# Kernel optimization log

Measured on AMD Instinct MI355X. Metric: run time of the kernel, lower is better.

Reference implementation:

```python
import jax, jax.numpy as jnp
import numpy as np

N_BUF = 60000.0
S_INIT = 2.0
S_INV = N_BUF ** S_INIT          # buffer init: N**S_init
S_HAT = (N_BUF ** 2) / S_INV     # == 1.0 at init


def setup_inputs() -> dict:
    key = jax.random.key(0)
    k1, k2 = jax.random.split(key)
    feats = jax.random.normal(k1, (16384, 128), dtype=jnp.float32)
    idx = jax.random.randint(k2, (16384,), 0, 60000).astype(jnp.int64)
    return {"feats": feats, "idx": idx}


def reference(feats, idx):
    # CauchyLoss.forward, faithful to the torch source. Note: the original
    # uses out-of-place masked_fill whose result is discarded, so neither the
    # diagonal nor the positive pairs are zeroed before the row-sum; we
    # replicate that exactly.
    n = feats.shape[0]
    B = n // 2
    sq = jnp.sum(feats * feats, axis=1)                      # [2B]
    d2 = sq[:, None] + sq[None, :] - 2.0 * (feats @ feats.T)  # [2B, 2B]
    d2 = jnp.maximum(d2, 0.0)
    q = 1.0 / (d2 + 1.0)                                      # [2B, 2B]
    # positive pairs: pos_mask = roll(eye(2B), B, dims=1) -> (i, (i+B) % 2B)
    rows = jnp.arange(n)
    qii = q[rows, (rows + B) % n]                             # [2B]
    attractive = -jnp.log(qii)
    repulsive = jnp.log(jnp.sum(q, axis=1)) * S_HAT           # [2B]
    return attractive.mean() + repulsive.mean()
```

## Files before the change

### kernel.cpp

```cpp
#include <hip/hip_runtime.h>
#include <hip/hip_bf16.h>

#define N 16384
#define D 128
#define NTI 128
#define GBLK 2112
#define B_HALF 8192

typedef __attribute__((ext_vector_type(8))) short short8;
typedef __attribute__((ext_vector_type(4))) float f32x4;

__device__ inline unsigned short f2bf(float x) {
    union { float f; unsigned u; } c; c.f = x;
    unsigned r = c.u + 0x7fffu + ((c.u >> 16) & 1u);
    return (unsigned short)(r >> 16);
}

__global__ __launch_bounds__(256)
void prep_kernel(const float* __restrict__ feats, unsigned short* __restrict__ fbP,
                 float* __restrict__ sq, float* __restrict__ rsum,
                 float* __restrict__ qii) {
    const int g  = blockIdx.x * 256 + threadIdx.x;
    const int p  = g >> 3;
    const int t8 = g & 7;
    const int i0 = p, i1 = p + B_HALF;
    const float4* ra = reinterpret_cast<const float4*>(feats + (size_t)i0 * D + t8 * 16);
    const float4* rb = reinterpret_cast<const float4*>(feats + (size_t)i1 * D + t8 * 16);
    char* da = (char*)fbP + (size_t)(i0 >> 7) * 32768 + (size_t)(i0 & 127) * 16;
    char* db = (char*)fbP + (size_t)(i1 >> 7) * 32768 + (size_t)(i1 & 127) * 16;
    float sa = 0.f, sb = 0.f, dot = 0.f;
#pragma unroll
    for (int c = 0; c < 2; ++c) {
        float4 x0 = ra[2 * c], x1 = ra[2 * c + 1];
        float4 y0 = rb[2 * c], y1 = rb[2 * c + 1];
        sa  += x0.x * x0.x + x0.y * x0.y + x0.z * x0.z + x0.w * x0.w
             + x1.x * x1.x + x1.y * x1.y + x1.z * x1.z + x1.w * x1.w;
        sb  += y0.x * y0.x + y0.y * y0.y + y0.z * y0.z + y0.w * y0.w
             + y1.x * y1.x + y1.y * y1.y + y1.z * y1.z + y1.w * y1.w;
        dot += x0.x * y0.x + x0.y * y0.y + x0.z * y0.z + x0.w * y0.w
             + x1.x * y1.x + x1.y * y1.y + x1.z * y1.z + x1.w * y1.w;
        short8 ca, cb;
        ca[0] = f2bf(x0.x); ca[1] = f2bf(x0.y); ca[2] = f2bf(x0.z); ca[3] = f2bf(x0.w);
        ca[4] = f2bf(x1.x); ca[5] = f2bf(x1.y); ca[6] = f2bf(x1.z); ca[7] = f2bf(x1.w);
        cb[0] = f2bf(y0.x); cb[1] = f2bf(y0.y); cb[2] = f2bf(y0.z); cb[3] = f2bf(y0.w);
        cb[4] = f2bf(y1.x); cb[5] = f2bf(y1.y); cb[6] = f2bf(y1.z); cb[7] = f2bf(y1.w);
        *reinterpret_cast<short8*>(da + (2 * t8 + c) * 2048) = ca;
        *reinterpret_cast<short8*>(db + (2 * t8 + c) * 2048) = cb;
    }
    sa  += __shfl_xor(sa, 1);  sa  += __shfl_xor(sa, 2);  sa  += __shfl_xor(sa, 4);
    sb  += __shfl_xor(sb, 1);  sb  += __shfl_xor(sb, 2);  sb  += __shfl_xor(sb, 4);
    dot += __shfl_xor(dot, 1); dot += __shfl_xor(dot, 2); dot += __shfl_xor(dot, 4);
    if (t8 == 0) {
        sq[i0] = sa; sq[i1] = sb;
        rsum[i0] = 0.f; rsum[i1] = 0.f;
        float d2 = fmaxf(sa + sb - 2.f * dot, 0.f);
        float q = 1.f / (d2 + 1.f);
        qii[i0] = q; qii[i1] = q;
    }
}

__device__ __forceinline__ void stage_panel(unsigned short* dst, const char* src,
                                            int wid, int lane) {
#pragma unroll
    for (int it = 0; it < 8; ++it) {
        const int lbase = it * 4096 + wid * 1024;
        __builtin_amdgcn_global_load_lds(
            (const __attribute__((address_space(1))) void*)(src + lbase + lane * 16),
            (__attribute__((address_space(3))) void*)((char*)dst + lbase), 16, 0, 0);
    }
}

__global__ __launch_bounds__(256, 2)
void gram_kernel(const unsigned short* __restrict__ fbP, const float* __restrict__ sq,
                 float* __restrict__ rsum) {
    __shared__ __align__(16) unsigned short lB[2][16 * 128 * 8];

    const int bid = (blockIdx.x & 7) * (GBLK / 8) + (blockIdx.x >> 3);

    int u = (int)((130.0f - sqrtf(16900.0f - 8.0f * (float)bid)) * 0.25f);
    if (u < 0) u = 0; if (u > 31) u = 31;
    while (u > 0 && 2 * u * (65 - u) > bid) --u;
    while (2 * (u + 1) * (64 - u) <= bid) ++u;
    int rem = bid - 2 * u * (65 - u);
    const int cnt = 32 - u;
    int sub = 0;
    while (rem >= cnt) { rem -= cnt; ++sub; }
    const int ti  = 4 * u + sub;
    const int tj0 = ti + 4 * rem;
    const int nt  = (NTI - tj0 < 4) ? (NTI - tj0) : 4;

    const int tid  = threadIdx.x;
    const int lane = tid & 63;
    const int wid  = tid >> 6;
    const int wr   = wid >> 1, wc = wid & 1;
    const int lrow = lane & 15;
    const int lk   = lane >> 4;

    const char* pa = (const char*)fbP + (size_t)ti * 32768;
    short8 a[4][4];
#pragma unroll
    for (int kk = 0; kk < 4; ++kk)
#pragma unroll
        for (int m = 0; m < 4; ++m)
            a[kk][m] = *reinterpret_cast<const short8*>(
                pa + (kk * 4 + lk) * 2048 + (wr * 64 + m * 16 + lrow) * 16);

    float sqa[4][4];
#pragma unroll
    for (int m = 0; m < 4; ++m) {
        const float4 v = *reinterpret_cast<const float4*>(
            sq + ti * 128 + wr * 64 + m * 16 + lk * 4);
        sqa[m][0] = v.x; sqa[m][1] = v.y; sqa[m][2] = v.z; sqa[m][3] = v.w;
    }
    float sqb1[4][4];
#pragma unroll
    for (int t = 0; t < 4; ++t)
        if (t < nt)
#pragma unroll
            for (int n = 0; n < 4; ++n)
                sqb1[t][n] = sq[(tj0 + t) * 128 + wc * 64 + n * 16 + lrow] + 1.0f;

    float racc[4][4];
#pragma unroll
    for (int m = 0; m < 4; ++m)
#pragma unroll
        for (int r = 0; r < 4; ++r) racc[m][r] = 0.f;

    stage_panel(lB[0], (const char*)fbP + (size_t)tj0 * 32768, wid, lane);

#pragma unroll
    for (int t = 0; t < 4; ++t) {
        if (t < nt) {
            if (t == 0) asm volatile("s_waitcnt vmcnt(0)" ::: "memory");
            else        asm volatile("s_waitcnt vmcnt(4)" ::: "memory");
            __builtin_amdgcn_sched_barrier(0);
            __builtin_amdgcn_s_barrier();

            if (t + 1 < nt)
                stage_panel(lB[(t + 1) & 1],
                            (const char*)fbP + (size_t)(tj0 + t + 1) * 32768, wid, lane);

            const char* lbuf = (const char*)lB[t & 1];
            f32x4 acc[4][4];
#pragma unroll
            for (int m = 0; m < 4; ++m)
#pragma unroll
                for (int n = 0; n < 4; ++n) acc[m][n] = (f32x4){0.f, 0.f, 0.f, 0.f};
#pragma unroll
            for (int kk = 0; kk < 4; ++kk) {
                short8 b[4];
#pragma unroll
                for (int n = 0; n < 4; ++n)
                    b[n] = *reinterpret_cast<const short8*>(
                        lbuf + (kk * 4 + lk) * 2048 + (wc * 64 + n * 16 + lrow) * 16);
#pragma unroll
                for (int m = 0; m < 4; ++m)
#pragma unroll
                    for (int n = 0; n < 4; ++n)
                        acc[m][n] = __builtin_amdgcn_mfma_f32_16x16x32_bf16(
                            a[kk][m], b[n], acc[m][n], 0, 0, 0);
            }

            float cloc[4] = {0.f, 0.f, 0.f, 0.f};
#pragma unroll
            for (int m = 0; m < 4; ++m)
#pragma unroll
                for (int n = 0; n < 4; ++n)
#pragma unroll
                    for (int r = 0; r < 4; ++r) {
                        float x = fmaf(-2.f, acc[m][n][r], sqa[m][r]);
                        float q = __builtin_amdgcn_rcpf(fmaxf(x + sqb1[t][n], 1.0f));
                        racc[m][r] += q;
                        cloc[n] += q;
                    }
            if (tj0 + t != ti) {
#pragma unroll
                for (int n = 0; n < 4; ++n) {
                    float v = cloc[n];
                    v += __shfl_xor(v, 16);
                    v += __shfl_xor(v, 32);
                    if (lane < 16)
                        atomicAdd(&rsum[(tj0 + t) * 128 + wc * 64 + n * 16 + lrow], v);
                }
            }
        }
    }

#pragma unroll
    for (int m = 0; m < 4; ++m)
#pragma unroll
        for (int r = 0; r < 4; ++r) {
            float v = racc[m][r];
            v += __shfl_xor(v, 1);
            v += __shfl_xor(v, 2);
            v += __shfl_xor(v, 4);
            v += __shfl_xor(v, 8);
            if (lrow == 0)
                atomicAdd(&rsum[ti * 128 + wr * 64 + m * 16 + lk * 4 + r], v);
        }
}

__global__ __launch_bounds__(256)
void finish1_kernel(const float* __restrict__ rsum, const float* __restrict__ qii,
                    float* __restrict__ partial) {
    __shared__ float red[4];
    const int i = blockIdx.x * 256 + threadIdx.x;
    float v = __logf(rsum[i]) - __logf(qii[i]);
#pragma unroll
    for (int m = 32; m >= 1; m >>= 1) v += __shfl_xor(v, m);
    if ((threadIdx.x & 63) == 0) red[threadIdx.x >> 6] = v;
    __syncthreads();
    if (threadIdx.x == 0) partial[blockIdx.x] = red[0] + red[1] + red[2] + red[3];
}

__global__ __launch_bounds__(64)
void finish2_kernel(const float* __restrict__ partial, unsigned* __restrict__ out) {
    float v = partial[threadIdx.x];
#pragma unroll
    for (int m = 32; m >= 1; m >>= 1) v += __shfl_xor(v, m);
    if (threadIdx.x == 0) {
        float val = v / (float)N;
        union { float f; unsigned u; } c; c.f = val;
        out[0] = (c.u & 0xFFFF0000u) | (unsigned)f2bf(val);
    }
}

extern "C" void kernel_launch(void* const* d_in, const int* in_sizes, int n_in,
                              void* d_out, int out_size, void* d_ws, size_t ws_size,
                              hipStream_t stream) {
    const float* feats = (const float*)d_in[0];
    char* ws = (char*)d_ws;
    unsigned short* fbP = (unsigned short*)ws;
    float* sq      = (float*)(ws + (size_t)N * D * 2);
    float* rsum    = (float*)(ws + (size_t)N * D * 2 + (size_t)N * 4);
    float* qii     = (float*)(ws + (size_t)N * D * 2 + (size_t)N * 8);
    float* partial = (float*)(ws + (size_t)N * D * 2 + (size_t)N * 12);

    hipLaunchKernelGGL(prep_kernel, dim3(256), dim3(256), 0, stream,
                       feats, fbP, sq, rsum, qii);
    hipLaunchKernelGGL(gram_kernel, dim3(GBLK), dim3(256), 0, stream,
                       fbP, sq, rsum);
    hipLaunchKernelGGL(finish1_kernel, dim3(64), dim3(256), 0, stream,
                       rsum, qii, partial);
    hipLaunchKernelGGL(finish2_kernel, dim3(1), dim3(64), 0, stream,
                       partial, (unsigned*)d_out);
}
```

Baseline: 91.31 us.

## Use 512-thread gram blocks with half-K panel staging and LDS column sums

Doubles the gram kernel block to 8 waves, so each wave owns a 32-row slice instead of 64 and holds half the A fragments and accumulators. The B panel is streamed in half-K chunks through a smaller double-buffered LDS area, and the per-tile sq values are loaded into LDS. Column partial sums are accumulated with LDS atomics and flushed to global once per block, and the MFMA loop is wrapped in s_setprio. The aim is higher occupancy and fewer global atomics, at the cost of twice as many barriers per tile and a full vmcnt(0) wait before each chunk.

```diff
diff --git a/kernel.cpp b/kernel.cpp
--- a/kernel.cpp
+++ b/kernel.cpp
@@ -59,21 +59,12 @@
     }
 }
 
-__device__ __forceinline__ void stage_panel(unsigned short* dst, const char* src,
-                                            int wid, int lane) {
-#pragma unroll
-    for (int it = 0; it < 8; ++it) {
-        const int lbase = it * 4096 + wid * 1024;
-        __builtin_amdgcn_global_load_lds(
-            (const __attribute__((address_space(1))) void*)(src + lbase + lane * 16),
-            (__attribute__((address_space(3))) void*)((char*)dst + lbase), 16, 0, 0);
-    }
-}
-
-__global__ __launch_bounds__(256, 2)
+__global__ __launch_bounds__(512, 4)
 void gram_kernel(const unsigned short* __restrict__ fbP, const float* __restrict__ sq,
                  float* __restrict__ rsum) {
-    __shared__ __align__(16) unsigned short lB[2][16 * 128 * 8];
+    __shared__ __align__(16) unsigned short lB[2][8 * 128 * 8];
+    __shared__ float cs[512];
+    __shared__ float sqL[512];
 
     const int bid = (blockIdx.x & 7) * (GBLK / 8) + (blockIdx.x >> 3);
 
@@ -92,102 +83,142 @@
     const int tid  = threadIdx.x;
     const int lane = tid & 63;
     const int wid  = tid >> 6;
-    const int wr   = wid >> 1, wc = wid & 1;
+    const int wr   = wid >> 1;
+    const int wc   = wid & 1;
     const int lrow = lane & 15;
     const int lk   = lane >> 4;
 
     const char* pa = (const char*)fbP + (size_t)ti * 32768;
-    short8 a[4][4];
+    short8 a[4][2];
 #pragma unroll
     for (int kk = 0; kk < 4; ++kk)
 #pragma unroll
-        for (int m = 0; m < 4; ++m)
+        for (int m = 0; m < 2; ++m)
             a[kk][m] = *reinterpret_cast<const short8*>(
-                pa + (kk * 4 + lk) * 2048 + (wr * 64 + m * 16 + lrow) * 16);
-
-    float sqa[4][4];
-#pragma unroll
-    for (int m = 0; m < 4; ++m) {
+                pa + (kk * 4 + lk) * 2048 + (wr * 32 + m * 16 + lrow) * 16);
+
+    float sqa[2][4];
+#pragma unroll
+    for (int m = 0; m < 2; ++m) {
         const float4 v = *reinterpret_cast<const float4*>(
-            sq + ti * 128 + wr * 64 + m * 16 + lk * 4);
+            sq + ti * 128 + wr * 32 + m * 16 + lk * 4);
         sqa[m][0] = v.x; sqa[m][1] = v.y; sqa[m][2] = v.z; sqa[m][3] = v.w;
     }
-    float sqb1[4][4];
-#pragma unroll
-    for (int t = 0; t < 4; ++t)
-        if (t < nt)
-#pragma unroll
-            for (int n = 0; n < 4; ++n)
-                sqb1[t][n] = sq[(tj0 + t) * 128 + wc * 64 + n * 16 + lrow] + 1.0f;
-
-    float racc[4][4];
-#pragma unroll
-    for (int m = 0; m < 4; ++m)
+
+    cs[tid] = 0.f;
+    if (wid < 2) {
+        const char* ssrc = (const char*)(sq + tj0 * 128) + wid * 1024 + lane * 16;
+        __builtin_amdgcn_global_load_lds(
+            (const __attribute__((address_space(1))) void*)ssrc,
+            (__attribute__((address_space(3))) void*)((char*)sqL + wid * 1024 + lane * 16),
+            16, 0, 0);
+    }
+    {
+        const char* src = (const char*)fbP + (size_t)tj0 * 32768;
+#pragma unroll
+        for (int it = 0; it < 2; ++it) {
+            const int lbase = it * 8192 + wid * 1024;
+            __builtin_amdgcn_global_load_lds(
+                (const __attribute__((address_space(1))) void*)(src + lbase + lane * 16),
+                (__attribute__((address_space(3))) void*)((char*)lB[0] + lbase), 16, 0, 0);
+        }
+    }
+
+    float racc[2][4];
+#pragma unroll
+    for (int m = 0; m < 2; ++m)
 #pragma unroll
         for (int r = 0; r < 4; ++r) racc[m][r] = 0.f;
 
-    stage_panel(lB[0], (const char*)fbP + (size_t)tj0 * 32768, wid, lane);
-
-#pragma unroll
-    for (int t = 0; t < 4; ++t) {
-        if (t < nt) {
-            if (t == 0) asm volatile("s_waitcnt vmcnt(0)" ::: "memory");
-            else        asm volatile("s_waitcnt vmcnt(4)" ::: "memory");
-            __builtin_amdgcn_sched_barrier(0);
-            __builtin_amdgcn_s_barrier();
-
-            if (t + 1 < nt)
-                stage_panel(lB[(t + 1) & 1],
-                            (const char*)fbP + (size_t)(tj0 + t + 1) * 32768, wid, lane);
-
-            const char* lbuf = (const char*)lB[t & 1];
-            f32x4 acc[4][4];
-#pragma unroll
-            for (int m = 0; m < 4; ++m)
-#pragma unroll
-                for (int n = 0; n < 4; ++n) acc[m][n] = (f32x4){0.f, 0.f, 0.f, 0.f};
-#pragma unroll
-            for (int kk = 0; kk < 4; ++kk) {
+    __syncthreads();
+
+    f32x4 acc[2][4];
+
+#pragma unroll
+    for (int p = 0; p < 8; ++p) {
+        if (p < 2 * nt) {
+            if (p > 0) {
+                asm volatile("s_waitcnt vmcnt(0)" ::: "memory");
+                __builtin_amdgcn_sched_barrier(0);
+                __builtin_amdgcn_s_barrier();
+                __builtin_amdgcn_sched_barrier(0);
+            }
+            const int t = p >> 1, h = p & 1;
+
+            if (p + 1 < 2 * nt) {
+                const int t2 = (p + 1) >> 1, h2 = (p + 1) & 1;
+                const char* src = (const char*)fbP + (size_t)(tj0 + t2) * 32768 + h2 * 16384;
+                unsigned short* dst = lB[(p + 1) & 1];
+#pragma unroll
+                for (int it = 0; it < 2; ++it) {
+                    const int lbase = it * 8192 + wid * 1024;
+                    __builtin_amdgcn_global_load_lds(
+                        (const __attribute__((address_space(1))) void*)(src + lbase + lane * 16),
+                        (__attribute__((address_space(3))) void*)((char*)dst + lbase), 16, 0, 0);
+                }
+            }
+
+            if (h == 0) {
+#pragma unroll
+                for (int m = 0; m < 2; ++m)
+#pragma unroll
+                    for (int n = 0; n < 4; ++n) acc[m][n] = (f32x4){0.f, 0.f, 0.f, 0.f};
+            }
+
+            const char* lbuf = (const char*)lB[p & 1];
+            __builtin_amdgcn_s_setprio(1);
+#pragma unroll
+            for (int kh = 0; kh < 2; ++kh) {
+                const int kk = 2 * h + kh;
                 short8 b[4];
 #pragma unroll
                 for (int n = 0; n < 4; ++n)
                     b[n] = *reinterpret_cast<const short8*>(
-                        lbuf + (kk * 4 + lk) * 2048 + (wc * 64 + n * 16 + lrow) * 16);
-#pragma unroll
-                for (int m = 0; m < 4; ++m)
+                        lbuf + (kh * 4 + lk) * 2048 + (wc * 64 + n * 16 + lrow) * 16);
+#pragma unroll
+                for (int m = 0; m < 2; ++m)
 #pragma unroll
                     for (int n = 0; n < 4; ++n)
                         acc[m][n] = __builtin_amdgcn_mfma_f32_16x16x32_bf16(
                             a[kk][m], b[n], acc[m][n], 0, 0, 0);
             }
-
-            float cloc[4] = {0.f, 0.f, 0.f, 0.f};
-#pragma unroll
-            for (int m = 0; m < 4; ++m)
+            __builtin_amdgcn_s_setprio(0);
+
+            if (h == 1) {
+                float sqb1[4];
 #pragma unroll
                 for (int n = 0; n < 4; ++n)
-#pragma unroll
-                    for (int r = 0; r < 4; ++r) {
-                        float x = fmaf(-2.f, acc[m][n][r], sqa[m][r]);
-                        float q = __builtin_amdgcn_rcpf(fmaxf(x + sqb1[t][n], 1.0f));
-                        racc[m][r] += q;
-                        cloc[n] += q;
+                    sqb1[n] = sqL[t * 128 + wc * 64 + n * 16 + lrow] + 1.0f;
+                float cloc[4] = {0.f, 0.f, 0.f, 0.f};
+#pragma unroll
+                for (int m = 0; m < 2; ++m)
+#pragma unroll
+                    for (int n = 0; n < 4; ++n)
+#pragma unroll
+                        for (int r = 0; r < 4; ++r) {
+                            float x = fmaf(-2.f, acc[m][n][r], sqa[m][r]);
+                            float q = __builtin_amdgcn_rcpf(fmaxf(x + sqb1[n], 1.0f));
+                            racc[m][r] += q;
+                            cloc[n] += q;
+                        }
+                if (tj0 + t != ti) {
+#pragma unroll
+                    for (int n = 0; n < 4; ++n) {
+                        float v = cloc[n];
+                        v += __shfl_xor(v, 16);
+                        v += __shfl_xor(v, 32);
+                        if (lane < 16)
+                            atomicAdd(&cs[t * 128 + wc * 64 + n * 16 + lrow], v);
                     }
-            if (tj0 + t != ti) {
-#pragma unroll
-                for (int n = 0; n < 4; ++n) {
-                    float v = cloc[n];
-                    v += __shfl_xor(v, 16);
-                    v += __shfl_xor(v, 32);
-                    if (lane < 16)
-                        atomicAdd(&rsum[(tj0 + t) * 128 + wc * 64 + n * 16 + lrow], v);
                 }
             }
         }
     }
 
-#pragma unroll
-    for (int m = 0; m < 4; ++m)
+    __syncthreads();
+
+#pragma unroll
+    for (int m = 0; m < 2; ++m)
 #pragma unroll
         for (int r = 0; r < 4; ++r) {
             float v = racc[m][r];
@@ -196,8 +227,13 @@
             v += __shfl_xor(v, 4);
             v += __shfl_xor(v, 8);
             if (lrow == 0)
-                atomicAdd(&rsum[ti * 128 + wr * 64 + m * 16 + lk * 4 + r], v);
+                atomicAdd(&rsum[ti * 128 + wr * 32 + m * 16 + lk * 4 + r], v);
         }
+    {
+        const int t = tid >> 7, row = tid & 127;
+        if (t < nt && tj0 + t != ti)
+            atomicAdd(&rsum[(tj0 + t) * 128 + row], cs[tid]);
+    }
 }
 
 __global__ __launch_bounds__(256)
@@ -238,7 +274,7 @@
 
     hipLaunchKernelGGL(prep_kernel, dim3(256), dim3(256), 0, stream,
                        feats, fbP, sq, rsum, qii);
-    hipLaunchKernelGGL(gram_kernel, dim3(GBLK), dim3(256), 0, stream,
+    hipLaunchKernelGGL(gram_kernel, dim3(GBLK), dim3(512), 0, stream,
                        fbP, sq, rsum);
     hipLaunchKernelGGL(finish1_kernel, dim3(64), dim3(256), 0, stream,
                        rsum, qii, partial);
```

New measurement: 95.54 us. 1.05x slower.

## Split gram tiles into row halves and load B directly from global

Applied to the files above, without the earlier changes.

Each 128-row tile chunk is now split between two blocks that each handle 64 rows, doubling the grid and raising the occupancy hint to 4 blocks per CU. The LDS double-buffered staging of B panels is removed. A and B fragments are now read straight from global memory inside the k-loop instead of keeping A in registers and B in LDS. This reduces register and LDS pressure to improve occupancy and latency hiding, but it doubles global reads of the B panels, loses the explicit prefetch overlap, and adds more column atomics.

```diff
diff --git a/kernel.cpp b/kernel.cpp
--- a/kernel.cpp
+++ b/kernel.cpp
@@ -4,7 +4,8 @@
 #define N 16384
 #define D 128
 #define NTI 128
-#define GBLK 2112
+#define NCHUNK 2112
+#define GBLK2 4224
 #define B_HALF 8192
 
 typedef __attribute__((ext_vector_type(8))) short short8;
@@ -59,29 +60,18 @@
     }
 }
 
-__device__ __forceinline__ void stage_panel(unsigned short* dst, const char* src,
-                                            int wid, int lane) {
-#pragma unroll
-    for (int it = 0; it < 8; ++it) {
-        const int lbase = it * 4096 + wid * 1024;
-        __builtin_amdgcn_global_load_lds(
-            (const __attribute__((address_space(1))) void*)(src + lbase + lane * 16),
-            (__attribute__((address_space(3))) void*)((char*)dst + lbase), 16, 0, 0);
-    }
-}
-
-__global__ __launch_bounds__(256, 2)
+__global__ __launch_bounds__(256, 4)
 void gram_kernel(const unsigned short* __restrict__ fbP, const float* __restrict__ sq,
                  float* __restrict__ rsum) {
-    __shared__ __align__(16) unsigned short lB[2][16 * 128 * 8];
-
-    const int bid = (blockIdx.x & 7) * (GBLK / 8) + (blockIdx.x >> 3);
-
-    int u = (int)((130.0f - sqrtf(16900.0f - 8.0f * (float)bid)) * 0.25f);
+    const int bid  = (blockIdx.x & 7) * (GBLK2 / 8) + (blockIdx.x >> 3);
+    const int chnk = bid >> 1;
+    const int half = bid & 1;
+
+    int u = (int)((130.0f - sqrtf(16900.0f - 8.0f * (float)chnk)) * 0.25f);
     if (u < 0) u = 0; if (u > 31) u = 31;
-    while (u > 0 && 2 * u * (65 - u) > bid) --u;
-    while (2 * (u + 1) * (64 - u) <= bid) ++u;
-    int rem = bid - 2 * u * (65 - u);
+    while (u > 0 && 2 * u * (65 - u) > chnk) --u;
+    while (2 * (u + 1) * (64 - u) <= chnk) ++u;
+    int rem = chnk - 2 * u * (65 - u);
     const int cnt = 32 - u;
     int sub = 0;
     while (rem >= cnt) { rem -= cnt; ++sub; }
@@ -92,84 +82,71 @@
     const int tid  = threadIdx.x;
     const int lane = tid & 63;
     const int wid  = tid >> 6;
-    const int wr   = wid >> 1, wc = wid & 1;
+    const int wr   = wid >> 1;
+    const int wc   = wid & 1;
     const int lrow = lane & 15;
     const int lk   = lane >> 4;
+    const int row0 = half * 64 + wr * 32;
 
     const char* pa = (const char*)fbP + (size_t)ti * 32768;
-    short8 a[4][4];
-#pragma unroll
-    for (int kk = 0; kk < 4; ++kk)
-#pragma unroll
-        for (int m = 0; m < 4; ++m)
-            a[kk][m] = *reinterpret_cast<const short8*>(
-                pa + (kk * 4 + lk) * 2048 + (wr * 64 + m * 16 + lrow) * 16);
-
-    float sqa[4][4];
-#pragma unroll
-    for (int m = 0; m < 4; ++m) {
+    const int aoff0 = lk * 2048 + (row0 + lrow) * 16;
+    const int boff0 = lk * 2048 + (wc * 64 + lrow) * 16;
+
+    float sqa[2][4];
+#pragma unroll
+    for (int m = 0; m < 2; ++m) {
         const float4 v = *reinterpret_cast<const float4*>(
-            sq + ti * 128 + wr * 64 + m * 16 + lk * 4);
+            sq + ti * 128 + row0 + m * 16 + lk * 4);
         sqa[m][0] = v.x; sqa[m][1] = v.y; sqa[m][2] = v.z; sqa[m][3] = v.w;
     }
-    float sqb1[4][4];
-#pragma unroll
-    for (int t = 0; t < 4; ++t)
-        if (t < nt)
-#pragma unroll
-            for (int n = 0; n < 4; ++n)
-                sqb1[t][n] = sq[(tj0 + t) * 128 + wc * 64 + n * 16 + lrow] + 1.0f;
-
-    float racc[4][4];
-#pragma unroll
-    for (int m = 0; m < 4; ++m)
+
+    float racc[2][4];
+#pragma unroll
+    for (int m = 0; m < 2; ++m)
 #pragma unroll
         for (int r = 0; r < 4; ++r) racc[m][r] = 0.f;
-
-    stage_panel(lB[0], (const char*)fbP + (size_t)tj0 * 32768, wid, lane);
 
 #pragma unroll
     for (int t = 0; t < 4; ++t) {
         if (t < nt) {
-            if (t == 0) asm volatile("s_waitcnt vmcnt(0)" ::: "memory");
-            else        asm volatile("s_waitcnt vmcnt(4)" ::: "memory");
-            __builtin_amdgcn_sched_barrier(0);
-            __builtin_amdgcn_s_barrier();
-
-            if (t + 1 < nt)
-                stage_panel(lB[(t + 1) & 1],
-                            (const char*)fbP + (size_t)(tj0 + t + 1) * 32768, wid, lane);
-
-            const char* lbuf = (const char*)lB[t & 1];
-            f32x4 acc[4][4];
-#pragma unroll
-            for (int m = 0; m < 4; ++m)
+            const char* pb = (const char*)fbP + (size_t)(tj0 + t) * 32768;
+            float sqb1[4];
+#pragma unroll
+            for (int n = 0; n < 4; ++n)
+                sqb1[n] = sq[(tj0 + t) * 128 + wc * 64 + n * 16 + lrow] + 1.0f;
+
+            f32x4 acc[2][4];
+#pragma unroll
+            for (int m = 0; m < 2; ++m)
 #pragma unroll
                 for (int n = 0; n < 4; ++n) acc[m][n] = (f32x4){0.f, 0.f, 0.f, 0.f};
+
 #pragma unroll
             for (int kk = 0; kk < 4; ++kk) {
-                short8 b[4];
+                short8 av[2], bv[4];
+#pragma unroll
+                for (int m = 0; m < 2; ++m)
+                    av[m] = *reinterpret_cast<const short8*>(pa + aoff0 + kk * 8192 + m * 256);
 #pragma unroll
                 for (int n = 0; n < 4; ++n)
-                    b[n] = *reinterpret_cast<const short8*>(
-                        lbuf + (kk * 4 + lk) * 2048 + (wc * 64 + n * 16 + lrow) * 16);
-#pragma unroll
-                for (int m = 0; m < 4; ++m)
+                    bv[n] = *reinterpret_cast<const short8*>(pb + boff0 + kk * 8192 + n * 256);
+#pragma unroll
+                for (int m = 0; m < 2; ++m)
 #pragma unroll
                     for (int n = 0; n < 4; ++n)
                         acc[m][n] = __builtin_amdgcn_mfma_f32_16x16x32_bf16(
-                            a[kk][m], b[n], acc[m][n], 0, 0, 0);
+                            av[m], bv[n], acc[m][n], 0, 0, 0);
             }
 
             float cloc[4] = {0.f, 0.f, 0.f, 0.f};
 #pragma unroll
-            for (int m = 0; m < 4; ++m)
+            for (int m = 0; m < 2; ++m)
 #pragma unroll
                 for (int n = 0; n < 4; ++n)
 #pragma unroll
                     for (int r = 0; r < 4; ++r) {
                         float x = fmaf(-2.f, acc[m][n][r], sqa[m][r]);
-                        float q = __builtin_amdgcn_rcpf(fmaxf(x + sqb1[t][n], 1.0f));
+                        float q = __builtin_amdgcn_rcpf(fmaxf(x + sqb1[n], 1.0f));
                         racc[m][r] += q;
                         cloc[n] += q;
                     }
@@ -187,7 +164,7 @@
     }
 
 #pragma unroll
-    for (int m = 0; m < 4; ++m)
+    for (int m = 0; m < 2; ++m)
 #pragma unroll
         for (int r = 0; r < 4; ++r) {
             float v = racc[m][r];
@@ -196,7 +173,7 @@
             v += __shfl_xor(v, 4);
             v += __shfl_xor(v, 8);
             if (lrow == 0)
-                atomicAdd(&rsum[ti * 128 + wr * 64 + m * 16 + lk * 4 + r], v);
+                atomicAdd(&rsum[ti * 128 + row0 + m * 16 + lk * 4 + r], v);
         }
 }
 
@@ -238,7 +215,7 @@
 
     hipLaunchKernelGGL(prep_kernel, dim3(256), dim3(256), 0, stream,
                        feats, fbP, sq, rsum, qii);
-    hipLaunchKernelGGL(gram_kernel, dim3(GBLK), dim3(256), 0, stream,
+    hipLaunchKernelGGL(gram_kernel, dim3(GBLK2), dim3(256), 0, stream,
                        fbP, sq, rsum);
     hipLaunchKernelGGL(finish1_kernel, dim3(64), dim3(256), 0, stream,
                        rsum, qii, partial);
```

After: 95.67 us. 4.8% more time.
